# Kernel optimization log

Measured on AMD Instinct MI355X. Metric: run time of the kernel, lower is better.

The kernel has to match this reference:

```python
import jax, jax.numpy as jnp
import numpy as np

N = 100000       # nodes
E = 1600000      # edges (avg degree 16)
F = 256          # input feature dim
UNITS = 256
DIM = UNITS // 2 # mean/var split
GAMMA = 1.0


def setup_inputs() -> dict:
    key = jax.random.key(0)
    k = jax.random.split(key, 6)
    features = jax.random.normal(k[0], (N, F), dtype=jnp.float32)
    kernel = jax.random.normal(k[1], (F, UNITS), dtype=jnp.float32) * (1.0 / np.sqrt(F))
    row = jnp.sort(jax.random.randint(k[2], (E,), 0, N, dtype=jnp.int32))
    col = jax.random.randint(k[3], (E,), 0, N, dtype=jnp.int32)
    # normalized-adjacency-like positive edge weights
    adj1_vals = jax.random.uniform(k[4], (E,), dtype=jnp.float32) * (1.0 / 16.0)
    adj2_vals = jax.random.uniform(k[5], (E,), dtype=jnp.float32) * (1.0 / 16.0)
    return dict(features=features, kernel=kernel, row=row, col=col,
                adj1_vals=adj1_vals, adj2_vals=adj2_vals)


def _spmm(row, col, vals, x, n):
    # sparse [n,n] @ dense [n,d] via gather + segment_sum
    return jax.ops.segment_sum(vals[:, None] * x[col], row, num_segments=n)


def reference(features, kernel, row, col, adj1_vals, adj2_vals):
    n = features.shape[0]
    h = features @ kernel                       # [N, UNITS]
    mean = jax.nn.elu(h[:, :DIM])               # [N, DIM]
    var = jax.nn.relu(h[:, DIM:])               # [N, DIM]
    kl = jnp.sum(0.5 * jnp.mean(mean * mean + var - jnp.log(1e-8 + var) - 1.0, axis=1))
    att = jnp.exp(-GAMMA * var)                 # [N, DIM]
    mean_agg = _spmm(row, col, adj1_vals, mean * att, n)
    var_agg = _spmm(row, col, adj2_vals, var * att * att, n)
    out = jnp.concatenate([mean_agg, var_agg], axis=1)  # [N, UNITS]
    # activation=None -> identity (keras linear activation)
    return out, kl
```

## Files before the change

kernel.cpp:

```cpp
#include <hip/hip_runtime.h>
#include <hip/hip_bf16.h>
#include <hip/hip_fp16.h>
#include <math.h>

#define FF 256
#define UU 256
#define DD 128
#define BMG 64
#define BKG 32
#define ALD 40

typedef short short8 __attribute__((ext_vector_type(8)));
typedef float f32x4  __attribute__((ext_vector_type(4)));

__device__ __forceinline__ unsigned short f2bf(float x) {
    unsigned int u = __float_as_uint(x);
    return (unsigned short)((u + 0x7fffu + ((u >> 16) & 1u)) >> 16);
}
__device__ __forceinline__ float bf2f(unsigned short b) {
    return __uint_as_float(((unsigned int)b) << 16);
}

__global__ __launch_bounds__(256)
void prep_b_kernel(const float* __restrict__ B,
                   unsigned short* __restrict__ Bth,
                   unsigned short* __restrict__ Btl) {
    __shared__ float tile[64][65];
    const int t  = threadIdx.x;
    const int k0 = (blockIdx.x & 3) * 64;
    const int n0 = (blockIdx.x >> 2) * 64;
    #pragma unroll
    for (int i = 0; i < 16; ++i) {
        int idx = t + 256 * i;
        int kk = idx >> 6, nn = idx & 63;
        tile[kk][nn] = B[(size_t)(k0 + kk) * UU + n0 + nn];
    }
    __syncthreads();
    #pragma unroll
    for (int i = 0; i < 16; ++i) {
        int idx = t + 256 * i;
        int nn = idx >> 6, kk = idx & 63;
        float b = tile[kk][nn];
        unsigned short hb = f2bf(b);
        unsigned short lb = f2bf(b - bf2f(hb));
        Bth[(size_t)(n0 + nn) * FF + k0 + kk] = hb;
        Btl[(size_t)(n0 + nn) * FF + k0 + kk] = lb;
    }
}

__global__ __launch_bounds__(256, 2)
void gemm_mfma_kernel(const float* __restrict__ A,
                      const unsigned short* __restrict__ Bth,
                      const unsigned short* __restrict__ Btl,
                      __half* __restrict__ xmv,
                      float* __restrict__ klpart,
                      int n) {
    __shared__ unsigned short Ah[BMG * ALD], Al[BMG * ALD];
    __shared__ unsigned short Bh[UU * ALD],  Bl[UU * ALD];
    __shared__ float kls[4];

    const int t    = threadIdx.x;
    const int lane = t & 63;
    const int w    = t >> 6;
    const int l15  = lane & 15;
    const int lk   = (lane >> 4) * 8;
    const int r0   = blockIdx.x * BMG;

    f32x4 acc[4][4];
    #pragma unroll
    for (int m = 0; m < 4; ++m)
        #pragma unroll
        for (int j = 0; j < 4; ++j)
            acc[m][j] = (f32x4){0.f, 0.f, 0.f, 0.f};

    const int arow  = t >> 2;
    const int akseg = (t & 3) * 8;
    int garow = r0 + arow; if (garow >= n) garow = n - 1;
    const float* aptr = A + (size_t)garow * FF + akseg;

    for (int kt = 0; kt < FF; kt += BKG) {
        float4 a0 = *(const float4*)(aptr + kt);
        float4 a1 = *(const float4*)(aptr + kt + 4);
        float av[8] = {a0.x, a0.y, a0.z, a0.w, a1.x, a1.y, a1.z, a1.w};
        short8 hv, lv;
        #pragma unroll
        for (int i = 0; i < 8; ++i) {
            unsigned short hb = f2bf(av[i]);
            unsigned short lb = f2bf(av[i] - bf2f(hb));
            hv[i] = (short)hb; lv[i] = (short)lb;
        }
        *(short8*)(Ah + arow * ALD + akseg) = hv;
        *(short8*)(Al + arow * ALD + akseg) = lv;
        #pragma unroll
        for (int p = 0; p < 4; ++p) {
            int slot = t + 256 * p;
            int nr = slot >> 2, ks = (slot & 3) * 8;
            *(short8*)(Bh + nr * ALD + ks) = *(const short8*)(Bth + (size_t)nr * FF + kt + ks);
            *(short8*)(Bl + nr * ALD + ks) = *(const short8*)(Btl + (size_t)nr * FF + kt + ks);
        }
        __syncthreads();

        short8 fah[4], fal[4], fbh[4], fbl[4];
        #pragma unroll
        for (int m = 0; m < 4; ++m) {
            int row = 16 * m + l15;
            fah[m] = *(const short8*)(Ah + row * ALD + lk);
            fal[m] = *(const short8*)(Al + row * ALD + lk);
        }
        #pragma unroll
        for (int j = 0; j < 4; ++j) {
            int nn = (j < 2) ? (32 * w + 16 * j + l15)
                             : (DD + 32 * w + 16 * (j - 2) + l15);
            fbh[j] = *(const short8*)(Bh + nn * ALD + lk);
            fbl[j] = *(const short8*)(Bl + nn * ALD + lk);
        }
        #pragma unroll
        for (int m = 0; m < 4; ++m)
            #pragma unroll
            for (int j = 0; j < 4; ++j) {
                acc[m][j] = __builtin_amdgcn_mfma_f32_16x16x32_bf16(fah[m], fbh[j], acc[m][j], 0, 0, 0);
                acc[m][j] = __builtin_amdgcn_mfma_f32_16x16x32_bf16(fal[m], fbh[j], acc[m][j], 0, 0, 0);
                acc[m][j] = __builtin_amdgcn_mfma_f32_16x16x32_bf16(fah[m], fbl[j], acc[m][j], 0, 0, 0);
            }
        __syncthreads();
    }

    float klsum = 0.f;
    const int rbase = (lane >> 4) * 4;
    #pragma unroll
    for (int m = 0; m < 4; ++m)
        #pragma unroll
        for (int reg = 0; reg < 4; ++reg) {
            const int gr = r0 + 16 * m + rbase + reg;
            if (gr < n) {
                #pragma unroll
                for (int j = 0; j < 2; ++j) {
                    float h1 = acc[m][j][reg];
                    float h2 = acc[m][j + 2][reg];
                    float mm = h1 > 0.f ? h1 : expm1f(h1);
                    float vv = h2 > 0.f ? h2 : 0.f;
                    klsum += mm * mm + vv - logf(1e-8f + vv) - 1.f;
                    float att = expf(-vv);
                    const int cm = 32 * w + 16 * j + l15;
                    xmv[(size_t)gr * UU + cm]      = __float2half(mm * att);
                    xmv[(size_t)gr * UU + cm + DD] = __float2half(vv * att * att);
                }
            }
        }

    #pragma unroll
    for (int off = 32; off > 0; off >>= 1)
        klsum += __shfl_down(klsum, off, 64);
    if (lane == 0) kls[w] = klsum;
    __syncthreads();
    if (t == 0) klpart[blockIdx.x] = kls[0] + kls[1] + kls[2] + kls[3];
}

__global__ __launch_bounds__(256)
void rowptr_kernel(const int* __restrict__ rowi, int* __restrict__ rowptr,
                   int n, int e) {
    const int r = blockIdx.x * 256 + threadIdx.x;
    if (r > n) return;
    int lo = 0, hi = e;
    while (lo < hi) { int mid = (lo + hi) >> 1; if (rowi[mid] < r) lo = mid + 1; else hi = mid; }
    rowptr[r] = lo;
}

__device__ __forceinline__ void fma4h(float4& a, float w, uint2 v) {
    __half2 p = *(__half2*)&v.x, q = *(__half2*)&v.y;
    float2 pf = __half22float2(p), qf = __half22float2(q);
    a.x = fmaf(w, pf.x, a.x); a.y = fmaf(w, pf.y, a.y);
    a.z = fmaf(w, qf.x, a.z); a.w = fmaf(w, qf.y, a.w);
}

__global__ __launch_bounds__(256)
void spmm_kernel(const int* __restrict__ rowptr,
                 const int* __restrict__ coli,
                 const float* __restrict__ w1,
                 const float* __restrict__ w2,
                 const __half* __restrict__ xmv,
                 float* __restrict__ out,
                 int n) {
    const int lane = threadIdx.x & 63;
    const int wv   = threadIdx.x >> 6;
    const int r    = blockIdx.x * 4 + wv;
    if (r >= n) return;

    const uint2* __restrict__ x2 = (const uint2*)xmv;
    const int lb = rowptr[r];
    const int ub = rowptr[r + 1];
    const float* __restrict__ wsrc = (lane < 32) ? w1 : w2;

    float4 a0 = make_float4(0.f,0.f,0.f,0.f), a1 = a0, a2 = a0, a3 = a0;
    int e = lb;
    for (; e + 4 <= ub; e += 4) {
        const int c0 = __builtin_nontemporal_load(coli + e);
        const int c1 = __builtin_nontemporal_load(coli + e + 1);
        const int c2 = __builtin_nontemporal_load(coli + e + 2);
        const int c3 = __builtin_nontemporal_load(coli + e + 3);
        const float w0 = __builtin_nontemporal_load(wsrc + e);
        const float w1v = __builtin_nontemporal_load(wsrc + e + 1);
        const float w2v = __builtin_nontemporal_load(wsrc + e + 2);
        const float w3v = __builtin_nontemporal_load(wsrc + e + 3);
        const uint2 v0 = x2[(size_t)c0 * 64 + lane];
        const uint2 v1 = x2[(size_t)c1 * 64 + lane];
        const uint2 v2 = x2[(size_t)c2 * 64 + lane];
        const uint2 v3 = x2[(size_t)c3 * 64 + lane];
        fma4h(a0, w0, v0); fma4h(a1, w1v, v1);
        fma4h(a2, w2v, v2); fma4h(a3, w3v, v3);
    }
    for (; e < ub; ++e) {
        const int c = coli[e];
        const float w = wsrc[e];
        fma4h(a0, w, x2[(size_t)c * 64 + lane]);
    }
    f32x4 res;
    res[0] = (a0.x + a1.x) + (a2.x + a3.x);
    res[1] = (a0.y + a1.y) + (a2.y + a3.y);
    res[2] = (a0.z + a1.z) + (a2.z + a3.z);
    res[3] = (a0.w + a1.w) + (a2.w + a3.w);
    __builtin_nontemporal_store(res, (f32x4*)out + (size_t)r * 64 + lane);
}

__global__ __launch_bounds__(256)
void klreduce_kernel(const float* __restrict__ klpart, int nparts,
                     float* __restrict__ dst) {
    __shared__ float tmp[4];
    const int t = threadIdx.x;
    float s = 0.f;
    for (int i = t; i < nparts; i += 256) s += klpart[i];
    #pragma unroll
    for (int off = 32; off > 0; off >>= 1)
        s += __shfl_down(s, off, 64);
    if ((t & 63) == 0) tmp[t >> 6] = s;
    __syncthreads();
    if (t == 0) dst[0] = (0.5f / (float)DD) * (tmp[0] + tmp[1] + tmp[2] + tmp[3]);
}

extern "C" void kernel_launch(void* const* d_in, const int* in_sizes, int n_in,
                              void* d_out, int out_size, void* d_ws, size_t ws_size,
                              hipStream_t stream) {
    const float* features = (const float*)d_in[0];
    const float* kernelW  = (const float*)d_in[1];
    const int*   row      = (const int*)d_in[2];
    const int*   col      = (const int*)d_in[3];
    const float* a1       = (const float*)d_in[4];
    const float* a2       = (const float*)d_in[5];
    float*       out      = (float*)d_out;

    const int n = in_sizes[0] / FF;
    const int e = in_sizes[2];

    __half*         xmv    = (__half*)d_ws;
    unsigned short* Bth    = (unsigned short*)(xmv + (size_t)n * UU);
    unsigned short* Btl    = Bth + (size_t)FF * UU;
    int*            rowptr = (int*)(Btl + (size_t)FF * UU);
    float*          klpart = (float*)(rowptr + n + 2);

    const int nblocks = (n + BMG - 1) / BMG;

    prep_b_kernel<<<16, 256, 0, stream>>>(kernelW, Bth, Btl);
    gemm_mfma_kernel<<<nblocks, 256, 0, stream>>>(features, Bth, Btl, xmv, klpart, n);
    rowptr_kernel<<<(n + 256) / 256, 256, 0, stream>>>(row, rowptr, n, e);
    spmm_kernel<<<(n + 3) / 4, 256, 0, stream>>>(rowptr, col, a1, a2, xmv, out, n);
    klreduce_kernel<<<1, 256, 0, stream>>>(klpart, nblocks, out + (size_t)n * UU);
}
```

Measured before the change: 392.0 us.

## Prefetch GEMM tiles into registers and split SpMM rows across two waves

The GEMM now loads the next K-tile of A and B into registers while the MFMAs run on the current tile, overlapping global loads with compute. The SpMM assigns two waves per row, each taking half the edges, and combines the two partial sums through shared memory. Column indices and weights are loaded once per 64 edges with coalesced lane loads and then broadcast with shuffles, replacing the scalar per-edge loads. The costs are more registers in the GEMM, a block-wide barrier and LDS traffic in the SpMM, and shuffle overhead on each edge.

```diff
diff --git a/kernel.cpp b/kernel.cpp
--- a/kernel.cpp
+++ b/kernel.cpp
@@ -78,27 +78,53 @@
     int garow = r0 + arow; if (garow >= n) garow = n - 1;
     const float* aptr = A + (size_t)garow * FF + akseg;
 
+    float4 pa0, pa1;
+    short8 pbh[4], pbl[4];
+
+    pa0 = *(const float4*)(aptr + 0);
+    pa1 = *(const float4*)(aptr + 4);
+    #pragma unroll
+    for (int p = 0; p < 4; ++p) {
+        int slot = t + 256 * p;
+        int nr = slot >> 2, ks = (slot & 3) * 8;
+        pbh[p] = *(const short8*)(Bth + (size_t)nr * FF + 0 + ks);
+        pbl[p] = *(const short8*)(Btl + (size_t)nr * FF + 0 + ks);
+    }
+
     for (int kt = 0; kt < FF; kt += BKG) {
-        float4 a0 = *(const float4*)(aptr + kt);
-        float4 a1 = *(const float4*)(aptr + kt + 4);
-        float av[8] = {a0.x, a0.y, a0.z, a0.w, a1.x, a1.y, a1.z, a1.w};
-        short8 hv, lv;
-        #pragma unroll
-        for (int i = 0; i < 8; ++i) {
-            unsigned short hb = f2bf(av[i]);
-            unsigned short lb = f2bf(av[i] - bf2f(hb));
-            hv[i] = (short)hb; lv[i] = (short)lb;
-        }
-        *(short8*)(Ah + arow * ALD + akseg) = hv;
-        *(short8*)(Al + arow * ALD + akseg) = lv;
-        #pragma unroll
-        for (int p = 0; p < 4; ++p) {
-            int slot = t + 256 * p;
-            int nr = slot >> 2, ks = (slot & 3) * 8;
-            *(short8*)(Bh + nr * ALD + ks) = *(const short8*)(Bth + (size_t)nr * FF + kt + ks);
-            *(short8*)(Bl + nr * ALD + ks) = *(const short8*)(Btl + (size_t)nr * FF + kt + ks);
+        {
+            float av[8] = {pa0.x, pa0.y, pa0.z, pa0.w, pa1.x, pa1.y, pa1.z, pa1.w};
+            short8 hv, lv;
+            #pragma unroll
+            for (int i = 0; i < 8; ++i) {
+                unsigned short hb = f2bf(av[i]);
+                unsigned short lb = f2bf(av[i] - bf2f(hb));
+                hv[i] = (short)hb; lv[i] = (short)lb;
+            }
+            *(short8*)(Ah + arow * ALD + akseg) = hv;
+            *(short8*)(Al + arow * ALD + akseg) = lv;
+            #pragma unroll
+            for (int p = 0; p < 4; ++p) {
+                int slot = t + 256 * p;
+                int nr = slot >> 2, ks = (slot & 3) * 8;
+                *(short8*)(Bh + nr * ALD + ks) = pbh[p];
+                *(short8*)(Bl + nr * ALD + ks) = pbl[p];
+            }
         }
         __syncthreads();
+
+        const int kt2 = kt + BKG;
+        if (kt2 < FF) {
+            pa0 = *(const float4*)(aptr + kt2);
+            pa1 = *(const float4*)(aptr + kt2 + 4);
+            #pragma unroll
+            for (int p = 0; p < 4; ++p) {
+                int slot = t + 256 * p;
+                int nr = slot >> 2, ks = (slot & 3) * 8;
+                pbh[p] = *(const short8*)(Bth + (size_t)nr * FF + kt2 + ks);
+                pbl[p] = *(const short8*)(Btl + (size_t)nr * FF + kt2 + ks);
+            }
+        }
 
         short8 fah[4], fal[4], fbh[4], fbl[4];
         #pragma unroll
@@ -181,45 +207,78 @@
                  const __half* __restrict__ xmv,
                  float* __restrict__ out,
                  int n) {
+    __shared__ float red[2][64][4];
+
     const int lane = threadIdx.x & 63;
     const int wv   = threadIdx.x >> 6;
-    const int r    = blockIdx.x * 4 + wv;
-    if (r >= n) return;
+    const int rl   = wv >> 1;
+    const int half = wv & 1;
+    const int r    = blockIdx.x * 2 + rl;
+    const bool valid = r < n;
+    const int rr   = valid ? r : (n - 1);
+
+    const int lb  = rowptr[rr];
+    const int ub  = rowptr[rr + 1];
+    const int deg = ub - lb;
+    const int hl  = (deg + 1) >> 1;
+    const int start = lb + (half ? hl : 0);
+    const int cnt   = half ? (deg - hl) : hl;
 
     const uint2* __restrict__ x2 = (const uint2*)xmv;
-    const int lb = rowptr[r];
-    const int ub = rowptr[r + 1];
-    const float* __restrict__ wsrc = (lane < 32) ? w1 : w2;
-
     float4 a0 = make_float4(0.f,0.f,0.f,0.f), a1 = a0, a2 = a0, a3 = a0;
-    int e = lb;
-    for (; e + 4 <= ub; e += 4) {
-        const int c0 = __builtin_nontemporal_load(coli + e);
-        const int c1 = __builtin_nontemporal_load(coli + e + 1);
-        const int c2 = __builtin_nontemporal_load(coli + e + 2);
-        const int c3 = __builtin_nontemporal_load(coli + e + 3);
-        const float w0 = __builtin_nontemporal_load(wsrc + e);
-        const float w1v = __builtin_nontemporal_load(wsrc + e + 1);
-        const float w2v = __builtin_nontemporal_load(wsrc + e + 2);
-        const float w3v = __builtin_nontemporal_load(wsrc + e + 3);
-        const uint2 v0 = x2[(size_t)c0 * 64 + lane];
-        const uint2 v1 = x2[(size_t)c1 * 64 + lane];
-        const uint2 v2 = x2[(size_t)c2 * 64 + lane];
-        const uint2 v3 = x2[(size_t)c3 * 64 + lane];
-        fma4h(a0, w0, v0); fma4h(a1, w1v, v1);
-        fma4h(a2, w2v, v2); fma4h(a3, w3v, v3);
-    }
-    for (; e < ub; ++e) {
-        const int c = coli[e];
-        const float w = wsrc[e];
-        fma4h(a0, w, x2[(size_t)c * 64 + lane]);
-    }
-    f32x4 res;
-    res[0] = (a0.x + a1.x) + (a2.x + a3.x);
-    res[1] = (a0.y + a1.y) + (a2.y + a3.y);
-    res[2] = (a0.z + a1.z) + (a2.z + a3.z);
-    res[3] = (a0.w + a1.w) + (a2.w + a3.w);
-    __builtin_nontemporal_store(res, (f32x4*)out + (size_t)r * 64 + lane);
+
+    for (int base = start; base < start + cnt; base += 64) {
+        const int m = min(64, start + cnt - base);
+        const int   ce = (lane < m) ? coli[base + lane] : 0;
+        const float wa = (lane < m) ? w1[base + lane]   : 0.f;
+        const float wb = (lane < m) ? w2[base + lane]   : 0.f;
+
+        int i = 0;
+        for (; i + 4 <= m; i += 4) {
+            const int c0 = __shfl(ce, i),     c1 = __shfl(ce, i + 1);
+            const int c2 = __shfl(ce, i + 2), c3 = __shfl(ce, i + 3);
+            const float wa0 = __shfl(wa, i),     wb0 = __shfl(wb, i);
+            const float wa1 = __shfl(wa, i + 1), wb1 = __shfl(wb, i + 1);
+            const float wa2 = __shfl(wa, i + 2), wb2 = __shfl(wb, i + 2);
+            const float wa3 = __shfl(wa, i + 3), wb3 = __shfl(wb, i + 3);
+            const float w0 = (lane < 32) ? wa0 : wb0;
+            const float w1v = (lane < 32) ? wa1 : wb1;
+            const float w2v = (lane < 32) ? wa2 : wb2;
+            const float w3v = (lane < 32) ? wa3 : wb3;
+            const uint2 v0 = x2[(size_t)c0 * 64 + lane];
+            const uint2 v1 = x2[(size_t)c1 * 64 + lane];
+            const uint2 v2 = x2[(size_t)c2 * 64 + lane];
+            const uint2 v3 = x2[(size_t)c3 * 64 + lane];
+            fma4h(a0, w0, v0);  fma4h(a1, w1v, v1);
+            fma4h(a2, w2v, v2); fma4h(a3, w3v, v3);
+        }
+        for (; i < m; ++i) {
+            const int c = __shfl(ce, i);
+            const float waw = __shfl(wa, i), wbw = __shfl(wb, i);
+            const float w = (lane < 32) ? waw : wbw;
+            fma4h(a0, w, x2[(size_t)c * 64 + lane]);
+        }
+    }
+
+    float4 s;
+    s.x = (a0.x + a1.x) + (a2.x + a3.x);
+    s.y = (a0.y + a1.y) + (a2.y + a3.y);
+    s.z = (a0.z + a1.z) + (a2.z + a3.z);
+    s.w = (a0.w + a1.w) + (a2.w + a3.w);
+
+    if (half == 1) {
+        red[rl][lane][0] = s.x; red[rl][lane][1] = s.y;
+        red[rl][lane][2] = s.z; red[rl][lane][3] = s.w;
+    }
+    __syncthreads();
+    if (half == 0 && valid) {
+        f32x4 res;
+        res[0] = s.x + red[rl][lane][0];
+        res[1] = s.y + red[rl][lane][1];
+        res[2] = s.z + red[rl][lane][2];
+        res[3] = s.w + red[rl][lane][3];
+        __builtin_nontemporal_store(res, (f32x4*)out + (size_t)r * 64 + lane);
+    }
 }
 
 __global__ __launch_bounds__(256)
@@ -262,6 +321,6 @@
     prep_b_kernel<<<16, 256, 0, stream>>>(kernelW, Bth, Btl);
     gemm_mfma_kernel<<<nblocks, 256, 0, stream>>>(features, Bth, Btl, xmv, klpart, n);
     rowptr_kernel<<<(n + 256) / 256, 256, 0, stream>>>(row, rowptr, n, e);
-    spmm_kernel<<<(n + 3) / 4, 256, 0, stream>>>(rowptr, col, a1, a2, xmv, out, n);
+    spmm_kernel<<<(n + 1) / 2, 256, 0, stream>>>(rowptr, col, a1, a2, xmv, out, n);
     klreduce_kernel<<<1, 256, 0, stream>>>(klpart, nblocks, out + (size_t)n * UU);
 }
```

Result: faster. 383.6 us (-2.1%).
